# Kernel tuning notes

Measured on AMD Instinct MI355X. Metric: run time of the kernel, lower is better.

## Reference

```python
import jax, jax.numpy as jnp
import numpy as np

N = 50000
E = 800000
IN_DIM = 128
HID = 64
HEADS = 4
OUT_DIM = 121
NEG_SLOPE = 0.2
EPS = 1e-16


def setup_inputs() -> dict:
    key = jax.random.key(0)
    ks = jax.random.split(key, 16)
    glorot = lambda k, shape: jax.random.normal(k, shape, jnp.float32) * (2.0 / (shape[0] + shape[-1])) ** 0.5
    HC = HEADS * HID
    return {
        "x": jax.random.normal(ks[0], (N, IN_DIM), jnp.float32),
        "edge_index": jax.random.randint(ks[1], (2, E), 0, N, jnp.int64),
        # conv1: GATConv(IN_DIM -> HID, heads=HEADS, concat)
        "W1": glorot(ks[2], (IN_DIM, HC)),
        "att_src1": glorot(ks[3], (HEADS, HID)),
        "att_dst1": glorot(ks[4], (HEADS, HID)),
        "b1": jnp.zeros((HC,), jnp.float32),
        # conv2: GATConv(HC -> HID, heads=HEADS, concat)
        "W2": glorot(ks[5], (HC, HC)),
        "att_src2": glorot(ks[6], (HEADS, HID)),
        "att_dst2": glorot(ks[7], (HEADS, HID)),
        "b2": jnp.zeros((HC,), jnp.float32),
        # post_mp: Linear(HC, HID) -> Dropout -> Linear(HID, OUT_DIM)
        "Wm1": glorot(ks[8], (HC, HID)),
        "bm1": jnp.zeros((HID,), jnp.float32),
        "Wm2": glorot(ks[9], (HID, OUT_DIM)),
        "bm2": jnp.zeros((OUT_DIM,), jnp.float32),
    }


def gat_conv(x, src, dst, W, att_src, att_dst, b):
    """PyG GATConv (concat=True, add_self_loops already applied to src/dst)."""
    n = x.shape[0]
    h = (x @ W).reshape(n, HEADS, -1)                     # [N, H, C]
    a_s = jnp.einsum("nhc,hc->nh", h, att_src)            # [N, H]
    a_d = jnp.einsum("nhc,hc->nh", h, att_dst)            # [N, H]
    e = jax.nn.leaky_relu(a_s[src] + a_d[dst], NEG_SLOPE)  # [Etot, H]
    # segment softmax over destination nodes
    m = jax.ops.segment_max(e, dst, num_segments=n)       # [N, H]
    ex = jnp.exp(e - m[dst])
    denom = jax.ops.segment_sum(ex, dst, num_segments=n)  # [N, H]
    alpha = ex / (denom[dst] + EPS)                        # [Etot, H]
    out = jax.ops.segment_sum(alpha[:, :, None] * h[src], dst, num_segments=n)  # [N, H, C]
    return out.reshape(n, -1) + b


def reference(x, edge_index, W1, att_src1, att_dst1, b1, W2, att_src2, att_dst2, b2, Wm1, bm1, Wm2, bm2):
    n = x.shape[0]
    loops = jnp.arange(n, dtype=edge_index.dtype)
    src = jnp.concatenate([edge_index[0], loops])
    dst = jnp.concatenate([edge_index[1], loops])
    h = jax.nn.relu(gat_conv(x, src, dst, W1, att_src1, att_dst1, b1))
    h = jax.nn.relu(gat_conv(h, src, dst, W2, att_src2, att_dst2, b2))
    h = h @ Wm1 + bm1
    h = h @ Wm2 + bm2
    return jax.nn.sigmoid(h)
```

## Files before the change

### kernel.cpp

```cpp
#include <hip/hip_runtime.h>
#include <hip/hip_bf16.h>
#include <float.h>

#define HEADS 4
#define HID 64
#define HC 256
#define NEG_SLOPE 0.2f
#define EPS 1e-16f
#define SLOG 7
#define SLOTS 128

typedef short bf16x8 __attribute__((ext_vector_type(8)));
typedef float f32x4 __attribute__((ext_vector_type(4)));
typedef unsigned short ushort8 __attribute__((ext_vector_type(8)));

__device__ __forceinline__ float bflo(unsigned u) { return __uint_as_float(u << 16); }
__device__ __forceinline__ float bfhi(unsigned u) { return __uint_as_float(u & 0xffff0000u); }
__device__ __forceinline__ unsigned packbf2(float a, float b) {
  __hip_bfloat16 ha = __float2bfloat16(a), hb = __float2bfloat16(b);
  unsigned short ua = *reinterpret_cast<unsigned short*>(&ha);
  unsigned short ub = *reinterpret_cast<unsigned short*>(&hb);
  return (unsigned)ua | ((unsigned)ub << 16);
}

#define PK 40

__global__ void __launch_bounds__(256) conv_gemm_attn(
    const __hip_bfloat16* __restrict__ A, const __hip_bfloat16* __restrict__ Bt,
    __hip_bfloat16* __restrict__ Cb,
    const float* __restrict__ att_s, const float* __restrict__ att_d,
    float* __restrict__ a_s, float* __restrict__ a_d,
    float* __restrict__ blockmax, int M, int K) {
  __shared__ unsigned short As[2][64 * PK];
  __shared__ unsigned short Bs[2][256 * PK];
  int tid = threadIdx.x;
  int lane = tid & 63, w = tid >> 6;
  int col16 = lane & 15, quad = lane >> 4;
  int row0 = blockIdx.x * 64;
  const unsigned short* Ag = (const unsigned short*)A;
  const unsigned short* Bg = (const unsigned short*)Bt;

  int ar = tid >> 2;
  int ako = (tid & 3) << 3;
  int agr = row0 + ar; if (agr >= M) agr = M - 1;
  const unsigned short* aga = Ag + (size_t)agr * K + ako;

  f32x4 acc[4][4] = {};
  int niter = K >> 5;

  ushort8 pa, pb[4];
  pa = *(const ushort8*)(aga);
#pragma unroll
  for (int p = 0; p < 4; p++) {
    int i2 = tid + (p << 8);
    int br = i2 >> 2, bko = (i2 & 3) << 3;
    pb[p] = *(const ushort8*)(Bg + (size_t)br * K + bko);
  }
  *(ushort8*)(&As[0][ar * PK + ako]) = pa;
#pragma unroll
  for (int p = 0; p < 4; p++) {
    int i2 = tid + (p << 8);
    int br = i2 >> 2, bko = (i2 & 3) << 3;
    *(ushort8*)(&Bs[0][br * PK + bko]) = pb[p];
  }
  __syncthreads();

  for (int it = 0; it < niter; ++it) {
    int cur = it & 1, nxt = cur ^ 1;
    int k1 = (it + 1) << 5;
    if (it + 1 < niter) {
      pa = *(const ushort8*)(aga + k1);
#pragma unroll
      for (int p = 0; p < 4; p++) {
        int i2 = tid + (p << 8);
        int br = i2 >> 2, bko = (i2 & 3) << 3;
        pb[p] = *(const ushort8*)(Bg + (size_t)br * K + k1 + bko);
      }
    }
    bf16x8 a[4], b[4];
#pragma unroll
    for (int i = 0; i < 4; i++)
      a[i] = *(const bf16x8*)(&As[cur][(i * 16 + col16) * PK + quad * 8]);
#pragma unroll
    for (int j = 0; j < 4; j++)
      b[j] = *(const bf16x8*)(&Bs[cur][((w << 6) + j * 16 + col16) * PK + quad * 8]);
#pragma unroll
    for (int i = 0; i < 4; i++)
#pragma unroll
      for (int j = 0; j < 4; j++)
        acc[i][j] = __builtin_amdgcn_mfma_f32_16x16x32_bf16(a[i], b[j], acc[i][j], 0, 0, 0);
    if (it + 1 < niter) {
      *(ushort8*)(&As[nxt][ar * PK + ako]) = pa;
#pragma unroll
      for (int p = 0; p < 4; p++) {
        int i2 = tid + (p << 8);
        int br = i2 >> 2, bko = (i2 & 3) << 3;
        *(ushort8*)(&Bs[nxt][br * PK + bko]) = pb[p];
      }
    }
    __syncthreads();
  }

#pragma unroll
  for (int i = 0; i < 4; i++) {
#pragma unroll
    for (int j = 0; j < 4; j++) {
      int gc = (w << 6) + j * 16 + col16;
      int grb = row0 + i * 16 + quad * 4;
#pragma unroll
      for (int r = 0; r < 4; r++) {
        int gr = grb + r;
        if (gr < M) Cb[(size_t)gr * 256 + gc] = __float2bfloat16(acc[i][j][r]);
      }
    }
  }

  float ws4[4], wd4[4];
#pragma unroll
  for (int j = 0; j < 4; j++) {
    ws4[j] = att_s[(w << 6) + j * 16 + col16];
    wd4[j] = att_d[(w << 6) + j * 16 + col16];
  }
  float wavemax = -FLT_MAX;
#pragma unroll
  for (int i = 0; i < 4; i++) {
#pragma unroll
    for (int r = 0; r < 4; r++) {
      float vs = 0.f, vd = 0.f;
#pragma unroll
      for (int j = 0; j < 4; j++) {
        vs += acc[i][j][r] * ws4[j];
        vd += acc[i][j][r] * wd4[j];
      }
#pragma unroll
      for (int off = 1; off < 16; off <<= 1) {
        vs += __shfl_xor(vs, off);
        vd += __shfl_xor(vd, off);
      }
      int gr = row0 + i * 16 + quad * 4 + r;
      if (col16 == 0 && gr < M) {
        a_s[(size_t)gr * 4 + w] = vs;
        a_d[(size_t)gr * 4 + w] = vd;
      }
      wavemax = fmaxf(wavemax, vs);
    }
  }
  wavemax = fmaxf(wavemax, __shfl_xor(wavemax, 16));
  wavemax = fmaxf(wavemax, __shfl_xor(wavemax, 32));
  if (lane == 0) blockmax[(size_t)blockIdx.x * 4 + w] = wavemax;
}

__global__ void __launch_bounds__(256) reduce_gmax(const float* __restrict__ blockmax,
                                                   float* __restrict__ gmaxf, int goff, int nb) {
  __shared__ float wm[4][4];
  int tid = threadIdx.x, lane = tid & 63, w = tid >> 6;
  int hd = tid & 3;
  float m = -FLT_MAX;
  for (int i = tid >> 2; i < nb; i += 64)
    m = fmaxf(m, blockmax[(size_t)i * 4 + hd]);
#pragma unroll
  for (int off = 4; off < 64; off <<= 1)
    m = fmaxf(m, __shfl_xor(m, off));
  if (lane < 4) wm[w][lane] = m;
  __syncthreads();
  if (tid < 4) {
    float r = fmaxf(fmaxf(wm[0][tid], wm[1][tid]), fmaxf(wm[2][tid], wm[3][tid]));
    gmaxf[goff + tid] = r;
  }
}

#define TS 72

__global__ void __launch_bounds__(256) postmp_fused(
    const __hip_bfloat16* __restrict__ A, const __hip_bfloat16* __restrict__ Wm1t,
    const __hip_bfloat16* __restrict__ Wm2t, const float* __restrict__ bm1,
    const float* __restrict__ bm2, float* __restrict__ out, int M) {
  __shared__ unsigned short smem[24576];
  unsigned short* W2s = &smem[15360];
  int tid = threadIdx.x;
  int lane = tid & 63, w = tid >> 6;
  int col16 = lane & 15, quad = lane >> 4;
  int row0 = blockIdx.x * 128;
  const unsigned short* Ag = (const unsigned short*)A;
  const unsigned short* Bg = (const unsigned short*)Wm1t;
  const unsigned short* W2g = (const unsigned short*)Wm2t;

#pragma unroll
  for (int c = tid; c < 1024; c += 256) {
    int r = c >> 3, ko = (c & 7) << 3;
    ushort8 v = {};
    if (r < 121) v = *(const ushort8*)(W2g + (size_t)r * 64 + ko);
    *(ushort8*)(&W2s[r * TS + ko]) = v;
  }

  int ar0 = tid >> 2, ako = (tid & 3) << 3;
  int agr0 = row0 + ar0;       if (agr0 >= M) agr0 = M - 1;
  int agr1 = row0 + ar0 + 64;  if (agr1 >= M) agr1 = M - 1;
  const unsigned short* aga0 = Ag + (size_t)agr0 * 256 + ako;
  const unsigned short* aga1 = Ag + (size_t)agr1 * 256 + ako;
  int br = tid >> 2, bko = (tid & 3) << 3;
  const unsigned short* bga = Bg + (size_t)br * 256 + bko;

  f32x4 acc1[2][4] = {};
  ushort8 pa0, pa1, pbv;
  pa0 = *(const ushort8*)(aga0);
  pa1 = *(const ushort8*)(aga1);
  pbv = *(const ushort8*)(bga);
  *(ushort8*)(&smem[ar0 * PK + ako]) = pa0;
  *(ushort8*)(&smem[(ar0 + 64) * PK + ako]) = pa1;
  *(ushort8*)(&smem[10240 + br * PK + bko]) = pbv;
  __syncthreads();

  for (int it = 0; it < 8; ++it) {
    int cur = it & 1, nxt = cur ^ 1;
    unsigned short* Asc = &smem[cur * 5120];
    unsigned short* Bsc = &smem[10240 + cur * 2560];
    int k1 = (it + 1) << 5;
    if (it + 1 < 8) {
      pa0 = *(const ushort8*)(aga0 + k1);
      pa1 = *(const ushort8*)(aga1 + k1);
      pbv = *(const ushort8*)(bga + k1);
    }
    bf16x8 a[2], b[4];
#pragma unroll
    for (int i = 0; i < 2; i++)
      a[i] = *(const bf16x8*)(&Asc[(w * 32 + i * 16 + col16) * PK + quad * 8]);
#pragma unroll
    for (int j = 0; j < 4; j++)
      b[j] = *(const bf16x8*)(&Bsc[(j * 16 + col16) * PK + quad * 8]);
#pragma unroll
    for (int i = 0; i < 2; i++)
#pragma unroll
      for (int j = 0; j < 4; j++)
        acc1[i][j] = __builtin_amdgcn_mfma_f32_16x16x32_bf16(a[i], b[j], acc1[i][j], 0, 0, 0);
    if (it + 1 < 8) {
      unsigned short* Asn = &smem[nxt * 5120];
      unsigned short* Bsn = &smem[10240 + nxt * 2560];
      *(ushort8*)(&Asn[ar0 * PK + ako]) = pa0;
      *(ushort8*)(&Asn[(ar0 + 64) * PK + ako]) = pa1;
      *(ushort8*)(&Bsn[br * PK + bko]) = pbv;
    }
    __syncthreads();
  }

  unsigned short* T = &smem[0];
#pragma unroll
  for (int i = 0; i < 2; i++) {
#pragma unroll
    for (int j = 0; j < 4; j++) {
      int col = j * 16 + col16;
      float bv = bm1[col];
#pragma unroll
      for (int r = 0; r < 4; r++) {
        int rl = w * 32 + i * 16 + quad * 4 + r;
        __hip_bfloat16 hv = __float2bfloat16(acc1[i][j][r] + bv);
        T[rl * TS + col] = *reinterpret_cast<unsigned short*>(&hv);
      }
    }
  }
  __syncthreads();

  int wm2 = w & 1, wn2 = w >> 1;
  f32x4 acc2[4][4] = {};
#pragma unroll
  for (int kk = 0; kk < 2; kk++) {
    bf16x8 a[4], b[4];
#pragma unroll
    for (int i = 0; i < 4; i++)
      a[i] = *(const bf16x8*)(&T[(wm2 * 64 + i * 16 + col16) * TS + kk * 32 + quad * 8]);
#pragma unroll
    for (int j = 0; j < 4; j++)
      b[j] = *(const bf16x8*)(&W2s[(wn2 * 64 + j * 16 + col16) * TS + kk * 32 + quad * 8]);
#pragma unroll
    for (int i = 0; i < 4; i++)
#pragma unroll
      for (int j = 0; j < 4; j++)
        acc2[i][j] = __builtin_amdgcn_mfma_f32_16x16x32_bf16(a[i], b[j], acc2[i][j], 0, 0, 0);
  }
#pragma unroll
  for (int i = 0; i < 4; i++) {
#pragma unroll
    for (int j = 0; j < 4; j++) {
      int gc = wn2 * 64 + j * 16 + col16;
      if (gc >= 121) continue;
      float bv = bm2[gc];
      int grb = row0 + wm2 * 64 + i * 16 + quad * 4;
#pragma unroll
      for (int r = 0; r < 4; r++) {
        int gr = grb + r;
        if (gr >= M) continue;
        float v = acc2[i][j][r] + bv;
        out[(size_t)gr * 121 + gc] = 1.f / (1.f + __expf(-v));
      }
    }
  }
}

__global__ void setup_all(const float* __restrict__ x, __hip_bfloat16* __restrict__ xb,
                          const float* __restrict__ W1, const float* __restrict__ W2,
                          const float* __restrict__ Wm1, const float* __restrict__ Wm2,
                          __hip_bfloat16* __restrict__ W1t, __hip_bfloat16* __restrict__ W2t,
                          __hip_bfloat16* __restrict__ Wm1t, __hip_bfloat16* __restrict__ Wm2t,
                          int* __restrict__ cur, int* __restrict__ slots,
                          int n, int castBlocks, int prepBlocks) {
  int b = blockIdx.x;
  int tid = threadIdx.x;
  if (b < castBlocks) {
    int i = b * 256 + tid;
    if (i < n * 32) {
      float4 v = *(const float4*)(x + 4 * (size_t)i);
      uint2 pk;
      pk.x = packbf2(v.x, v.y);
      pk.y = packbf2(v.z, v.w);
      *(uint2*)((unsigned*)xb + 2 * (size_t)i) = pk;
    }
    return;
  }
  b -= castBlocks;
  if (b < prepBlocks) {
    int i = b * 256 + tid;
    if (i < 128 * 256) {
      int nn = i / 128, kk = i - nn * 128;
      W1t[i] = __float2bfloat16(W1[(size_t)kk * 256 + nn]);
      return;
    }
    i -= 128 * 256;
    if (i < 256 * 256) {
      int nn = i / 256, kk = i - nn * 256;
      W2t[i] = __float2bfloat16(W2[(size_t)kk * 256 + nn]);
      return;
    }
    i -= 256 * 256;
    if (i < 256 * 64) {
      int nn = i / 256, kk = i - nn * 256;
      Wm1t[i] = __float2bfloat16(Wm1[(size_t)kk * 64 + nn]);
      return;
    }
    i -= 256 * 64;
    if (i < 64 * 121) {
      int nn = i / 64, kk = i - nn * 64;
      Wm2t[i] = __float2bfloat16(Wm2[(size_t)kk * 121 + nn]);
    }
    return;
  }
  b -= prepBlocks;
  {
    int i = b * 256 + tid;
    if (i < n) {
      cur[i] = 1;
      slots[(size_t)i << SLOG] = i;
    }
  }
}

__global__ void slot_fill(const int* __restrict__ ei, int E,
                          int* __restrict__ cur, int* __restrict__ slots) {
  int i = blockIdx.x * 256 + threadIdx.x;
  if (i >= E) return;
  int s = ei[i], d = ei[E + i];
  int pos = atomicAdd(&cur[d], 1);
  slots[((size_t)d << SLOG) + pos] = s;
}

__global__ void __launch_bounds__(256) gat_aggregate(
    const __hip_bfloat16* __restrict__ hb, const float* __restrict__ a_src,
    const float* __restrict__ a_dst, const int* __restrict__ cnt_arr,
    const int* __restrict__ slots, const float* __restrict__ bias,
    const float* __restrict__ gmaxf, int goff,
    __hip_bfloat16* __restrict__ out, int n) {
  __shared__ float plds[4][256];
  int wid = threadIdx.x >> 6;
  int lane = threadIdx.x & 63;
  int half = lane >> 5;
  int l32 = lane & 31;
  int qh = l32 >> 3;
  int node = (blockIdx.x << 2) + wid;
  if (node >= n) return;
  float4 adv = *(const float4*)(a_dst + (size_t)node * 4);
  float m0 = gmaxf[goff + 0] + adv.x; m0 = fmaxf(m0, NEG_SLOPE * m0);
  float m1 = gmaxf[goff + 1] + adv.y; m1 = fmaxf(m1, NEG_SLOPE * m1);
  float m2 = gmaxf[goff + 2] + adv.z; m2 = fmaxf(m2, NEG_SLOPE * m2);
  float m3 = gmaxf[goff + 3] + adv.w; m3 = fmaxf(m3, NEG_SLOPE * m3);
  int cntN = __builtin_amdgcn_readfirstlane(cnt_arr[node]);
  int beg = node << SLOG;
  const uint4* hw4 = (const uint4*)hb;

  float lq = 0.f;
  float c0 = 0.f, c1 = 0.f, c2 = 0.f, c3 = 0.f;
  float c4 = 0.f, c5 = 0.f, c6 = 0.f, c7 = 0.f;

  for (int cbeg = 0; cbeg < cntN; cbeg += 64) {
    int cnt = cntN - cbeg; if (cnt > 64) cnt = 64;
    int eidx = beg + cbeg + (lane < cnt ? lane : cnt - 1);
    int s_l = slots[eidx];
    float4 as = *(const float4*)(a_src + (size_t)s_l * 4);
    float v0 = as.x + adv.x; v0 = fmaxf(v0, NEG_SLOPE * v0);
    float v1 = as.y + adv.y; v1 = fmaxf(v1, NEG_SLOPE * v1);
    float v2 = as.z + adv.z; v2 = fmaxf(v2, NEG_SLOPE * v2);
    float v3 = as.w + adv.w; v3 = fmaxf(v3, NEG_SLOPE * v3);
    float p0 = __expf(v0 - m0), p1 = __expf(v1 - m1);
    float p2 = __expf(v2 - m2), p3 = __expf(v3 - m3);
    *(float4*)&plds[wid][lane * 4] = make_float4(p0, p1, p2, p3);
    __builtin_amdgcn_s_waitcnt(0);

    auto step = [&](int j) {
      int jj = j + half;
      bool dup = jj >= cnt;
      int jc = dup ? cnt - 1 : jj;
      int sj = __shfl(s_l, jc);
      float pq = plds[wid][jc * 4 + qh];
      if (dup) pq = 0.f;
      uint4 d = hw4[(size_t)sj * 32 + l32];
      c0 += pq * bflo(d.x); c1 += pq * bfhi(d.x);
      c2 += pq * bflo(d.y); c3 += pq * bfhi(d.y);
      c4 += pq * bflo(d.z); c5 += pq * bfhi(d.z);
      c6 += pq * bflo(d.w); c7 += pq * bfhi(d.w);
      lq += pq;
    };
    for (int j = 0; j < cnt; j += 8) { step(j); step(j + 2); step(j + 4); step(j + 6); }
  }

  lq += __shfl_xor(lq, 32);
  c0 += __shfl_xor(c0, 32); c1 += __shfl_xor(c1, 32);
  c2 += __shfl_xor(c2, 32); c3 += __shfl_xor(c3, 32);
  c4 += __shfl_xor(c4, 32); c5 += __shfl_xor(c5, 32);
  c6 += __shfl_xor(c6, 32); c7 += __shfl_xor(c7, 32);

  if (half == 0) {
    float4 bA = *(const float4*)(bias + 8 * l32);
    float4 bB = *(const float4*)(bias + 8 * l32 + 4);
    float rq = 1.f / (lq + EPS);
    float o0 = fmaxf(c0 * rq + bA.x, 0.f);
    float o1 = fmaxf(c1 * rq + bA.y, 0.f);
    float o2 = fmaxf(c2 * rq + bA.z, 0.f);
    float o3 = fmaxf(c3 * rq + bA.w, 0.f);
    float o4 = fmaxf(c4 * rq + bB.x, 0.f);
    float o5 = fmaxf(c5 * rq + bB.y, 0.f);
    float o6 = fmaxf(c6 * rq + bB.z, 0.f);
    float o7 = fmaxf(c7 * rq + bB.w, 0.f);
    uint4 pk;
    pk.x = packbf2(o0, o1);
    pk.y = packbf2(o2, o3);
    pk.z = packbf2(o4, o5);
    pk.w = packbf2(o6, o7);
    *(uint4*)((unsigned*)out + (size_t)node * 128 + l32 * 4) = pk;
  }
}

extern "C" void kernel_launch(void* const* d_in, const int* in_sizes, int n_in,
                              void* d_out, int out_size, void* d_ws, size_t ws_size,
                              hipStream_t stream) {
  const float* x      = (const float*)d_in[0];
  const int*   ei     = (const int*)d_in[1];
  const float* W1     = (const float*)d_in[2];
  const float* att_s1 = (const float*)d_in[3];
  const float* att_d1 = (const float*)d_in[4];
  const float* b1     = (const float*)d_in[5];
  const float* W2     = (const float*)d_in[6];
  const float* att_s2 = (const float*)d_in[7];
  const float* att_d2 = (const float*)d_in[8];
  const float* b2     = (const float*)d_in[9];
  const float* Wm1    = (const float*)d_in[10];
  const float* bm1    = (const float*)d_in[11];
  const float* Wm2    = (const float*)d_in[12];
  const float* bm2    = (const float*)d_in[13];
  float* out = (float*)d_out;

  int n = in_sizes[0] / 128;
  int E = in_sizes[1] / 2;

  char* ws = (char*)d_ws;
  size_t off = 0;
  auto carve = [&](size_t bytes) {
    char* p = ws + off;
    off += (bytes + 255) & ~(size_t)255;
    return p;
  };
  __hip_bfloat16* hb   = (__hip_bfloat16*)carve((size_t)n * HC * 2);
  __hip_bfloat16* aggb = (__hip_bfloat16*)carve((size_t)n * HC * 2);
  __hip_bfloat16* xb   = (__hip_bfloat16*)carve((size_t)n * 128 * 2);
  __hip_bfloat16* W1t  = (__hip_bfloat16*)carve((size_t)128 * HC * 2);
  __hip_bfloat16* W2t  = (__hip_bfloat16*)carve((size_t)HC * HC * 2);
  __hip_bfloat16* Wm1t = (__hip_bfloat16*)carve((size_t)HC * HID * 2);
  __hip_bfloat16* Wm2t = (__hip_bfloat16*)carve((size_t)HID * 121 * 2);
  float* as    = (float*)carve((size_t)n * HEADS * 4);
  float* ad    = (float*)carve((size_t)n * HEADS * 4);
  int*   cur   = (int*)carve((size_t)n * 4);
  int*   slots = (int*)carve(((size_t)n << SLOG) * 4);
  float* blockmax = (float*)carve((size_t)((n + 63) / 64) * 4 * 4);
  float* gmaxf    = (float*)carve((size_t)8 * 4);
  (void)ws_size;

  int rows64 = (n + 63) / 64;
  int castBlocks = (n * 32 + 255) / 256;
  int prepBlocks = (122432 + 255) / 256;
  int slotBlocks = (n + 255) / 256;

  setup_all<<<castBlocks + prepBlocks + slotBlocks, 256, 0, stream>>>(
      x, xb, W1, W2, Wm1, Wm2, W1t, W2t, Wm1t, Wm2t, cur, slots,
      n, castBlocks, prepBlocks);
  slot_fill<<<(E + 255) / 256, 256, 0, stream>>>(ei, E, cur, slots);

  conv_gemm_attn<<<rows64, 256, 0, stream>>>(
      xb, W1t, hb, att_s1, att_d1, as, ad, blockmax, n, 128);
  reduce_gmax<<<1, 256, 0, stream>>>(blockmax, gmaxf, 0, rows64);
  gat_aggregate<<<(n + 3) / 4, 256, 0, stream>>>(hb, as, ad, cur, slots, b1, gmaxf, 0, aggb, n);

  conv_gemm_attn<<<rows64, 256, 0, stream>>>(
      aggb, W2t, hb, att_s2, att_d2, as, ad, blockmax, n, HC);
  reduce_gmax<<<1, 256, 0, stream>>>(blockmax, gmaxf, 4, rows64);
  gat_aggregate<<<(n + 3) / 4, 256, 0, stream>>>(hb, as, ad, cur, slots, b2, gmaxf, 4, aggb, n);

  postmp_fused<<<(n + 127) / 128, 256, 0, stream>>>(aggb, Wm1t, Wm2t, bm1, bm2, out, n);
}
```

Measured before the change: 362.5 us.

## Store projected features in column-sliced layout and aggregate per slice

The GEMM epilogue now writes the projected node features into eight 32-column slices, each stored contiguously across all nodes ([slice][node][32]), instead of row-major [node][256]. The aggregation kernel is split so that each block handles one slice for four nodes. The grid grows eightfold, so all blocks working on the same slice gather from a compact 3.2MB region that should stay cache-resident. Each wave handles 16 edges at a time with 4 lanes per edge. The cost is that per-edge source indices, attention logits and exponentials are recomputed eight times per node, plus a deeper cross-lane reduction.

```diff
diff --git a/kernel.cpp b/kernel.cpp
--- a/kernel.cpp
+++ b/kernel.cpp
@@ -106,11 +106,12 @@
 #pragma unroll
     for (int j = 0; j < 4; j++) {
       int gc = (w << 6) + j * 16 + col16;
+      size_t sbase = ((size_t)(gc >> 5) * M) * 32 + (gc & 31);
       int grb = row0 + i * 16 + quad * 4;
 #pragma unroll
       for (int r = 0; r < 4; r++) {
         int gr = grb + r;
-        if (gr < M) Cb[(size_t)gr * 256 + gc] = __float2bfloat16(acc[i][j][r]);
+        if (gr < M) Cb[sbase + (size_t)gr * 32] = __float2bfloat16(acc[i][j][r]);
       }
     }
   }
@@ -362,28 +363,26 @@
   slots[((size_t)d << SLOG) + pos] = s;
 }
 
-__global__ void __launch_bounds__(256) gat_aggregate(
-    const __hip_bfloat16* __restrict__ hb, const float* __restrict__ a_src,
-    const float* __restrict__ a_dst, const int* __restrict__ cnt_arr,
-    const int* __restrict__ slots, const float* __restrict__ bias,
-    const float* __restrict__ gmaxf, int goff,
+__global__ void __launch_bounds__(256) gat_aggregate_sl(
+    const __hip_bfloat16* __restrict__ hbs,
+    const float* __restrict__ a_src, const float* __restrict__ a_dst,
+    const int* __restrict__ cnt_arr, const int* __restrict__ slots,
+    const float* __restrict__ bias, const float* __restrict__ gmaxf, int goff,
     __hip_bfloat16* __restrict__ out, int n) {
-  __shared__ float plds[4][256];
-  int wid = threadIdx.x >> 6;
-  int lane = threadIdx.x & 63;
-  int half = lane >> 5;
-  int l32 = lane & 31;
-  int qh = l32 >> 3;
-  int node = (blockIdx.x << 2) + wid;
+  int tid = threadIdx.x;
+  int wid = tid >> 6, lane = tid & 63;
+  int slice = blockIdx.x & 7;
+  int node = ((blockIdx.x >> 3) << 2) + wid;
   if (node >= n) return;
-  float4 adv = *(const float4*)(a_dst + (size_t)node * 4);
-  float m0 = gmaxf[goff + 0] + adv.x; m0 = fmaxf(m0, NEG_SLOPE * m0);
-  float m1 = gmaxf[goff + 1] + adv.y; m1 = fmaxf(m1, NEG_SLOPE * m1);
-  float m2 = gmaxf[goff + 2] + adv.z; m2 = fmaxf(m2, NEG_SLOPE * m2);
-  float m3 = gmaxf[goff + 3] + adv.w; m3 = fmaxf(m3, NEG_SLOPE * m3);
+  int head = slice >> 1;
+  int lsub = lane & 3;
+  int egrp = lane >> 2;
+
+  float advh = a_dst[(size_t)node * 4 + head];
+  float mh = gmaxf[goff + head] + advh; mh = fmaxf(mh, NEG_SLOPE * mh);
   int cntN = __builtin_amdgcn_readfirstlane(cnt_arr[node]);
   int beg = node << SLOG;
-  const uint4* hw4 = (const uint4*)hb;
+  const uint4* hw4 = (const uint4*)hbs + (size_t)slice * n * 4 + lsub;
 
   float lq = 0.f;
   float c0 = 0.f, c1 = 0.f, c2 = 0.f, c3 = 0.f;
@@ -393,42 +392,36 @@
     int cnt = cntN - cbeg; if (cnt > 64) cnt = 64;
     int eidx = beg + cbeg + (lane < cnt ? lane : cnt - 1);
     int s_l = slots[eidx];
-    float4 as = *(const float4*)(a_src + (size_t)s_l * 4);
-    float v0 = as.x + adv.x; v0 = fmaxf(v0, NEG_SLOPE * v0);
-    float v1 = as.y + adv.y; v1 = fmaxf(v1, NEG_SLOPE * v1);
-    float v2 = as.z + adv.z; v2 = fmaxf(v2, NEG_SLOPE * v2);
-    float v3 = as.w + adv.w; v3 = fmaxf(v3, NEG_SLOPE * v3);
-    float p0 = __expf(v0 - m0), p1 = __expf(v1 - m1);
-    float p2 = __expf(v2 - m2), p3 = __expf(v3 - m3);
-    *(float4*)&plds[wid][lane * 4] = make_float4(p0, p1, p2, p3);
-    __builtin_amdgcn_s_waitcnt(0);
-
-    auto step = [&](int j) {
-      int jj = j + half;
-      bool dup = jj >= cnt;
-      int jc = dup ? cnt - 1 : jj;
+    float av = a_src[(size_t)s_l * 4 + head];
+    float v = av + advh; v = fmaxf(v, NEG_SLOPE * v);
+    float p_l = (lane < cnt) ? __expf(v - mh) : 0.f;
+
+    for (int j = 0; j < cnt; j += 16) {
+      int jc = j + egrp;
       int sj = __shfl(s_l, jc);
-      float pq = plds[wid][jc * 4 + qh];
-      if (dup) pq = 0.f;
-      uint4 d = hw4[(size_t)sj * 32 + l32];
+      float pq = __shfl(p_l, jc);
+      uint4 d = hw4[(size_t)sj * 4];
       c0 += pq * bflo(d.x); c1 += pq * bfhi(d.x);
       c2 += pq * bflo(d.y); c3 += pq * bfhi(d.y);
       c4 += pq * bflo(d.z); c5 += pq * bfhi(d.z);
       c6 += pq * bflo(d.w); c7 += pq * bfhi(d.w);
       lq += pq;
-    };
-    for (int j = 0; j < cnt; j += 8) { step(j); step(j + 2); step(j + 4); step(j + 6); }
-  }
-
-  lq += __shfl_xor(lq, 32);
-  c0 += __shfl_xor(c0, 32); c1 += __shfl_xor(c1, 32);
-  c2 += __shfl_xor(c2, 32); c3 += __shfl_xor(c3, 32);
-  c4 += __shfl_xor(c4, 32); c5 += __shfl_xor(c5, 32);
-  c6 += __shfl_xor(c6, 32); c7 += __shfl_xor(c7, 32);
-
-  if (half == 0) {
-    float4 bA = *(const float4*)(bias + 8 * l32);
-    float4 bB = *(const float4*)(bias + 8 * l32 + 4);
+    }
+  }
+
+#pragma unroll
+  for (int off = 4; off <= 32; off <<= 1) {
+    lq += __shfl_xor(lq, off);
+    c0 += __shfl_xor(c0, off); c1 += __shfl_xor(c1, off);
+    c2 += __shfl_xor(c2, off); c3 += __shfl_xor(c3, off);
+    c4 += __shfl_xor(c4, off); c5 += __shfl_xor(c5, off);
+    c6 += __shfl_xor(c6, off); c7 += __shfl_xor(c7, off);
+  }
+
+  if (lane < 4) {
+    int cb = slice * 32 + lane * 8;
+    float4 bA = *(const float4*)(bias + cb);
+    float4 bB = *(const float4*)(bias + cb + 4);
     float rq = 1.f / (lq + EPS);
     float o0 = fmaxf(c0 * rq + bA.x, 0.f);
     float o1 = fmaxf(c1 * rq + bA.y, 0.f);
@@ -443,7 +436,7 @@
     pk.y = packbf2(o2, o3);
     pk.z = packbf2(o4, o5);
     pk.w = packbf2(o6, o7);
-    *(uint4*)((unsigned*)out + (size_t)node * 128 + l32 * 4) = pk;
+    *(uint4*)((unsigned*)out + (size_t)node * 128 + (cb >> 1)) = pk;
   }
 }
 
@@ -495,6 +488,7 @@
   int castBlocks = (n * 32 + 255) / 256;
   int prepBlocks = (122432 + 255) / 256;
   int slotBlocks = (n + 255) / 256;
+  int aggBlocks = ((n + 3) / 4) * 8;
 
   setup_all<<<castBlocks + prepBlocks + slotBlocks, 256, 0, stream>>>(
       x, xb, W1, W2, Wm1, Wm2, W1t, W2t, Wm1t, Wm2t, cur, slots,
@@ -504,12 +498,12 @@
   conv_gemm_attn<<<rows64, 256, 0, stream>>>(
       xb, W1t, hb, att_s1, att_d1, as, ad, blockmax, n, 128);
   reduce_gmax<<<1, 256, 0, stream>>>(blockmax, gmaxf, 0, rows64);
-  gat_aggregate<<<(n + 3) / 4, 256, 0, stream>>>(hb, as, ad, cur, slots, b1, gmaxf, 0, aggb, n);
+  gat_aggregate_sl<<<aggBlocks, 256, 0, stream>>>(hb, as, ad, cur, slots, b1, gmaxf, 0, aggb, n);
 
   conv_gemm_attn<<<rows64, 256, 0, stream>>>(
       aggb, W2t, hb, att_s2, att_d2, as, ad, blockmax, n, HC);
   reduce_gmax<<<1, 256, 0, stream>>>(blockmax, gmaxf, 4, rows64);
-  gat_aggregate<<<(n + 3) / 4, 256, 0, stream>>>(hb, as, ad, cur, slots, b2, gmaxf, 4, aggb, n);
+  gat_aggregate_sl<<<aggBlocks, 256, 0, stream>>>(hb, as, ad, cur, slots, b2, gmaxf, 4, aggb, n);
 
   postmp_fused<<<(n + 127) / 128, 256, 0, stream>>>(aggb, Wm1t, Wm2t, bm1, bm2, out, n);
 }
```

After: 570.4 us. 57.3% more time.
